# Optimization experiments

Hardware: AMD Instinct MI355X
Metric: run time of the kernel (lower is better)

Reference implementation:

```python
import jax, jax.numpy as jnp
import numpy as np

N = 8192   # nodes in each graph (N1 must equal N2: V is built from x1)
D = 512    # output_dim


def setup_inputs() -> dict:
    key = jax.random.key(0)
    k1, k2, kq, kk, kv = jax.random.split(key, 5)
    std = 1.0 / np.sqrt(D)
    return {
        "x1": jax.random.normal(k1, (N, D), dtype=jnp.float32),
        "x2": jax.random.normal(k2, (N, D), dtype=jnp.float32),
        "q": jax.random.uniform(kq, (D, D), dtype=jnp.float32, minval=-std, maxval=std),
        "k": jax.random.uniform(kk, (D, D), dtype=jnp.float32, minval=-std, maxval=std),
        "v": jax.random.uniform(kv, (D, D), dtype=jnp.float32, minval=-std, maxval=std),
    }


def reference(x1, x2, q, k, v):
    Q = x1 @ q                       # [N, D]
    V = x1 @ v                       # [N, D]  (note: V from x1, as in the original)
    K = x2 @ k                       # [N, D]
    e = jax.nn.leaky_relu(Q @ K.T, negative_slope=0.01)  # [N, N]
    attention = jax.nn.softmax(e, axis=-1)
    return attention @ V             # [N, D]
```

## Files before the change

kernel.cpp:

```cpp
#include <hip/hip_runtime.h>
#include <hip/hip_bf16.h>

typedef unsigned short u16;
typedef unsigned int u32;
typedef float floatx4 __attribute__((ext_vector_type(4)));
typedef _Float16 f16x8 __attribute__((ext_vector_type(8)));

#define NN 8192
#define DD 512
#define NPARTS 4
#define JCHUNK 2048
#define RB_PER_PART 64

__device__ __forceinline__ u16 f2h(float f) {
    _Float16 h = (_Float16)f;
    return __builtin_bit_cast(u16, h);
}
__device__ __forceinline__ float h2f(u16 u) {
    _Float16 h = __builtin_bit_cast(_Float16, u);
    return (float)h;
}

__device__ __forceinline__ void async16(const u16* g, u16* l) {
    __builtin_amdgcn_global_load_lds(
        (const __attribute__((address_space(1))) u32*)g,
        (__attribute__((address_space(3))) u32*)l, 16, 0, 0);
}

__global__ __launch_bounds__(256)
void prep_kernel(const float* __restrict__ x1, const float* __restrict__ x2,
                 const float* __restrict__ qw, const float* __restrict__ kw,
                 const float* __restrict__ vw,
                 u16* __restrict__ x1h, u16* __restrict__ x2h,
                 u16* __restrict__ qT, u16* __restrict__ kT,
                 u16* __restrict__ vT, int* __restrict__ cnt)
{
    const int t = blockIdx.x * 256 + threadIdx.x;
    const int stride = gridDim.x * 256;
    if (t < NPARTS) cnt[t] = 0;

    const int NQ = NN * DD / 4;
    for (int i = t; i < NQ; i += stride) {
        float4 f = ((const float4*)x1)[i];
        ushort4 h;
        h.x = f2h(f.x); h.y = f2h(f.y); h.z = f2h(f.z); h.w = f2h(f.w);
        ((ushort4*)x1h)[i] = h;
        f = ((const float4*)x2)[i];
        h.x = f2h(f.x); h.y = f2h(f.y); h.z = f2h(f.z); h.w = f2h(f.w);
        ((ushort4*)x2h)[i] = h;
    }
    const int NW = DD * DD;
    for (int i = t; i < NW; i += stride) {
        const int k = i >> 9, n = i & 511;
        qT[n * DD + k] = f2h(qw[i]);
        kT[n * DD + k] = f2h(kw[i]);
        vT[n * DD + k] = f2h(vw[i]);
    }
}

__global__ __launch_bounds__(256, 2)
void proj_kernel(const u16* __restrict__ x1h, const u16* __restrict__ x2h,
                 const u16* __restrict__ qT, const u16* __restrict__ kT,
                 const u16* __restrict__ vT,
                 u16* __restrict__ Qf, u16* __restrict__ Kf, u16* __restrict__ VT)
{
    const int which = blockIdx.z;
    const u16* A = (which == 1) ? x2h : x1h;
    const u16* W = (which == 0) ? qT : (which == 1 ? kT : vT);

    __shared__ u16 Ab[2][128 * 64];
    __shared__ u16 Wb[2][128 * 64];

    const int tid  = threadIdx.x;
    const int lane = tid & 63;
    const int wave = tid >> 6;
    const int l15  = lane & 15;
    const int quad = lane >> 4;
    const int wm   = (wave & 1) * 64;
    const int wn   = (wave >> 1) * 64;
    const int m0   = blockIdx.x * 128;
    const int n0   = blockIdx.y * 128;

    const int vrs = lane >> 3;
    const int vch = (lane & 7) ^ vrs;
    int sOff[4];
    for (int i = 0; i < 4; i++) {
        const int c = wave * 4 + i;
        sOff[i] = (c * 8 + vrs) * DD + vch * 8;
    }

    auto stage = [&](int buf, int k0) {
        const u16* a = A + (size_t)m0 * DD + k0;
        const u16* w = W + (size_t)n0 * DD + k0;
        u16* da = &Ab[buf][wave * 2048];
        u16* dw = &Wb[buf][wave * 2048];
        async16(a + sOff[0], da);
        async16(a + sOff[1], da + 512);
        async16(a + sOff[2], da + 1024);
        async16(a + sOff[3], da + 1536);
        async16(w + sOff[0], dw);
        async16(w + sOff[1], dw + 512);
        async16(w + sOff[2], dw + 1024);
        async16(w + sOff[3], dw + 1536);
        __builtin_amdgcn_sched_barrier(0);
    };

    floatx4 acc[4][4] = {};

    stage(0, 0);
    asm volatile("s_waitcnt vmcnt(0)" ::: "memory");
    __syncthreads();

    for (int t = 0; t < 8; t++) {
        if (t < 7) stage((t & 1) ^ 1, (t + 1) * 64);
        const int buf = t & 1;
        __builtin_amdgcn_s_setprio(1);
        for (int ks = 0; ks < 2; ks++) {
            f16x8 af[4], bf[4];
            for (int mi = 0; mi < 4; mi++) {
                const int row = wm + mi * 16 + l15;
                const int ch  = (ks * 4 + quad) ^ (l15 & 7);
                af[mi] = *(const f16x8*)&Ab[buf][row * 64 + ch * 8];
            }
            for (int ni = 0; ni < 4; ni++) {
                const int row = wn + ni * 16 + l15;
                const int ch  = (ks * 4 + quad) ^ (l15 & 7);
                bf[ni] = *(const f16x8*)&Wb[buf][row * 64 + ch * 8];
            }
            for (int mi = 0; mi < 4; mi++)
                for (int ni = 0; ni < 4; ni++)
                    acc[mi][ni] = __builtin_amdgcn_mfma_f32_16x16x32_f16(
                        af[mi], bf[ni], acc[mi][ni], 0, 0, 0);
        }
        __builtin_amdgcn_s_setprio(0);
        asm volatile("s_waitcnt vmcnt(0)" ::: "memory");
        __syncthreads();
    }

    for (int mi = 0; mi < 4; mi++)
        for (int ni = 0; ni < 4; ni++) {
            if (which == 2) {
                const int row0 = m0 + wm + mi * 16 + quad * 4;
                const int col  = n0 + wn + ni * 16 + l15;
                uint2 p;
                p.x = ((u32)f2h(acc[mi][ni][1]) << 16) | f2h(acc[mi][ni][0]);
                p.y = ((u32)f2h(acc[mi][ni][3]) << 16) | f2h(acc[mi][ni][2]);
                *(uint2*)&VT[(size_t)col * NN + row0] = p;
            } else {
                for (int r = 0; r < 4; r++) {
                    const int row = m0 + wm + mi * 16 + quad * 4 + r;
                    const int col = n0 + wn + ni * 16 + l15;
                    const u16 hv = f2h(acc[mi][ni][r]);
                    if (which == 0) Qf[(size_t)row * DD + col] = hv;
                    else            Kf[(size_t)row * DD + col] = hv;
                }
            }
        }
}

__global__ __launch_bounds__(512, 2)
void attn_kernel(const u16* __restrict__ Qf, const u16* __restrict__ Kf,
                 const u16* __restrict__ VT,
                 u16* __restrict__ Opart, float* __restrict__ Mp,
                 float* __restrict__ Lp, int* __restrict__ cnt)
{
    const int tid  = threadIdx.x;
    const int lane = tid & 63;
    const int wave = tid >> 6;
    const int w3   = wave & 3;
    const int wsel = wave >> 2;
    const int l15  = lane & 15;
    const int quad = lane >> 4;

    __shared__ u16 KV[6][8192];
    __shared__ u16 Ps[8][16 * 68];
    __shared__ int sPart, sRb;

    if (tid == 0) {
        u32 xcd;
        asm volatile("s_getreg_b32 %0, hwreg(HW_REG_XCC_ID)" : "=s"(xcd));
        xcd &= 3;
        int part = -1, rb = 0;
        for (int t = 0; t < 4; t++) {
            const int p = (xcd + t) & 3;
            const int idx = atomicAdd(&cnt[p], 1);
            if (idx < RB_PER_PART) { part = p; rb = idx; break; }
        }
        sPart = part; sRb = rb;
    }
    __syncthreads();
    const int part = sPart;
    const int rb   = sRb;
    if (part < 0) return;

    const int q0 = rb * 128 + wave * 16;

    f16x8 qf[16];
    for (int kk = 0; kk < 16; kk++)
        qf[kk] = *(const f16x8*)&Qf[(size_t)(q0 + l15) * DD + kk * 32 + quad * 8];

    floatx4 o[32] = {};
    float m_run[4], l_run[4];
    for (int r = 0; r < 4; r++) { m_run[r] = -1e30f; l_run[r] = 0.f; }

    const int j_begin = part * JCHUNK;
    const int j_end   = j_begin + JCHUNK;

    const int krow4  = lane >> 4;
    const int kpos16 = lane & 15;
    const int vrs    = lane >> 3;
    const int vch    = (lane & 7) ^ vrs;

    int kOff[4], vOff[4];
    for (int i = 0; i < 4; i++) {
        const int c    = w3 * 4 + i;
        const int krow = c * 4 + krow4;
        kOff[i] = krow * DD + (kpos16 ^ (krow & 7)) * 8;
        vOff[i] = (c * 8 + vrs) * NN + vch * 8;
    }

    auto stageK = [&](int dq, int j0, int slot) {
        const u16* b = Kf + (size_t)j0 * DD + dq * 128;
        u16* d = &KV[slot][w3 * 2048];
        async16(b + kOff[0], d);
        async16(b + kOff[1], d + 512);
        async16(b + kOff[2], d + 1024);
        async16(b + kOff[3], d + 1536);
        __builtin_amdgcn_sched_barrier(0);
    };
    auto stageV = [&](int dq, int j0, int slot) {
        const u16* b = VT + (size_t)dq * 128 * NN + j0;
        u16* d = &KV[slot][w3 * 2048];
        async16(b + vOff[0], d);
        async16(b + vOff[1], d + 512);
        async16(b + vOff[2], d + 1024);
        async16(b + vOff[3], d + 1536);
        __builtin_amdgcn_sched_barrier(0);
    };

    auto qkQ = [&](int rg, int dq, floatx4* s) {
        __builtin_amdgcn_s_setprio(1);
        for (int k8 = 0; k8 < 4; k8++)
            for (int nt = 0; nt < 4; nt++) {
                const int row = nt * 16 + l15;
                const int ch  = (k8 * 4 + quad) ^ (l15 & 7);
                f16x8 b = *(const f16x8*)&KV[rg][row * 128 + ch * 8];
                s[nt] = __builtin_amdgcn_mfma_f32_16x16x32_f16(qf[dq * 4 + k8], b, s[nt], 0, 0, 0);
            }
        __builtin_amdgcn_s_setprio(0);
    };
    auto pvQ = [&](int rg, int dq) {
        f16x8 pf0 = *(const f16x8*)&Ps[wave][l15 * 68 + quad * 8];
        f16x8 pf1 = *(const f16x8*)&Ps[wave][l15 * 68 + 32 + quad * 8];
        __builtin_amdgcn_s_setprio(1);
        for (int t = 0; t < 8; t++) {
            const int row = t * 16 + l15;
            const int c0  = quad ^ (l15 & 7);
            const int c1  = (4 + quad) ^ (l15 & 7);
            f16x8 b0 = *(const f16x8*)&KV[rg][row * 64 + c0 * 8];
            f16x8 b1 = *(const f16x8*)&KV[rg][row * 64 + c1 * 8];
            o[dq * 8 + t] = __builtin_amdgcn_mfma_f32_16x16x32_f16(pf0, b0, o[dq * 8 + t], 0, 0, 0);
            o[dq * 8 + t] = __builtin_amdgcn_mfma_f32_16x16x32_f16(pf1, b1, o[dq * 8 + t], 0, 0, 0);
        }
        __builtin_amdgcn_s_setprio(0);
    };

    auto pbar = [&]() {
        asm volatile("s_waitcnt vmcnt(4)" ::: "memory");
        asm volatile("s_barrier" ::: "memory");
    };
    auto wrap6 = [](int x) { return x >= 6 ? x - 6 : x; };

    if (wsel == 0) { stageK(0, j_begin, 0); stageK(2, j_begin, 2); }
    else           { stageK(1, j_begin, 1); stageK(3, j_begin, 3); }
    asm volatile("s_waitcnt vmcnt(0)" ::: "memory");
    asm volatile("s_barrier" ::: "memory");

    int sc = 4;

    for (int j0 = j_begin; j0 < j_end; j0 += 64) {
        const int jn = (j0 + 64 < j_end) ? j0 + 64 : j_begin;
        floatx4 s[4] = {};
        int sA, sB, cA, cB;

        sA = sc; sB = sc + 1; cA = wrap6(sc + 2); cB = cA + 1; sc = cA;
        if (wsel == 0) stageV(0, j0, sA); else stageV(1, j0, sB);
        qkQ(cA, 0, s);
        qkQ(cB, 1, s);
        pbar();

        sA = sc; sB = sc + 1; cA = wrap6(sc + 2); cB = cA + 1; sc = cA;
        if (wsel == 0) stageV(2, j0, sA); else stageV(3, j0, sB);
        qkQ(cA, 2, s);
        qkQ(cB, 3, s);

        for (int nt = 0; nt < 4; nt++)
            for (int r = 0; r < 4; r++) {
                float x = s[nt][r];
                s[nt][r] = x >= 0.f ? x : 0.01f * x;
            }
        float mt4[4];
        for (int r = 0; r < 4; r++)
            mt4[r] = fmaxf(fmaxf(s[0][r], s[1][r]), fmaxf(s[2][r], s[3][r]));
        for (int off = 1; off < 16; off <<= 1)
            for (int r = 0; r < 4; r++)
                mt4[r] = fmaxf(mt4[r], __shfl_xor(mt4[r], off));

        float alpha[4];
        for (int r = 0; r < 4; r++) {
            const float mnew = fmaxf(m_run[r], mt4[r]);
            alpha[r] = __expf(m_run[r] - mnew);
            m_run[r] = mnew;
        }
        float ls[4] = {0.f, 0.f, 0.f, 0.f};
        u16 pv[4][4];
        for (int nt = 0; nt < 4; nt++)
            for (int r = 0; r < 4; r++) {
                const float p = __expf(s[nt][r] - m_run[r]);
                ls[r] += p;
                pv[nt][r] = f2h(p);
            }
        for (int off = 1; off < 16; off <<= 1)
            for (int r = 0; r < 4; r++)
                ls[r] += __shfl_xor(ls[r], off);
        for (int r = 0; r < 4; r++)
            l_run[r] = l_run[r] * alpha[r] + ls[r];
        const bool need = (alpha[0] != 1.f) | (alpha[1] != 1.f) |
                          (alpha[2] != 1.f) | (alpha[3] != 1.f);
        if (__any(need))
            for (int i = 0; i < 32; i++)
                for (int r = 0; r < 4; r++)
                    o[i][r] *= alpha[r];

        for (int nt = 0; nt < 4; nt++)
            for (int r = 0; r < 4; r++)
                Ps[wave][(quad * 4 + r) * 68 + nt * 16 + l15] = pv[nt][r];
        asm volatile("s_waitcnt lgkmcnt(0)" ::: "memory");

        pbar();

        sA = sc; sB = sc + 1; cA = wrap6(sc + 2); cB = cA + 1; sc = cA;
        if (wsel == 0) stageK(0, jn, sA); else stageK(1, jn, sB);
        pvQ(cA, 0);
        pvQ(cB, 1);
        pbar();

        sA = sc; sB = sc + 1; cA = wrap6(sc + 2); cB = cA + 1; sc = cA;
        if (wsel == 0) stageK(2, jn, sA); else stageK(3, jn, sB);
        pvQ(cA, 2);
        pvQ(cB, 3);
        pbar();
    }

    asm volatile("s_waitcnt vmcnt(0)" ::: "memory");

    for (int i = 0; i < 32; i++)
        for (int r = 0; r < 4; r++) {
            const int row = q0 + quad * 4 + r;
            const int col = i * 16 + l15;
            Opart[((size_t)part * NN + row) * DD + col] = f2h(o[i][r]);
        }
    if (l15 == 0)
        for (int r = 0; r < 4; r++) {
            const int row = q0 + quad * 4 + r;
            Mp[part * NN + row] = m_run[r];
            Lp[part * NN + row] = l_run[r];
        }
}

__global__ __launch_bounds__(256)
void combine_kernel(const u16* __restrict__ Opart, const float* __restrict__ Mp,
                    const float* __restrict__ Lp, float* __restrict__ out)
{
    const int t   = blockIdx.x * 256 + threadIdx.x;
    const int row = t >> 6;
    const int c0  = (t & 63) * 8;

    float m[NPARTS], l[NPARTS];
    float M = -1e30f;
    for (int p = 0; p < NPARTS; p++) {
        m[p] = Mp[p * NN + row];
        l[p] = Lp[p * NN + row];
        M = fmaxf(M, m[p]);
    }
    float w[NPARTS], L = 0.f;
    for (int p = 0; p < NPARTS; p++) { w[p] = __expf(m[p] - M); L += w[p] * l[p]; }
    const float inv = 1.f / L;

    float acc[8] = {};
    for (int p = 0; p < NPARTS; p++) {
        f16x8 v = *(const f16x8*)&Opart[((size_t)p * NN + row) * DD + c0];
        for (int j = 0; j < 8; j++)
            acc[j] += w[p] * (float)v[j];
    }
    float4 o0, o1;
    o0.x = acc[0] * inv; o0.y = acc[1] * inv; o0.z = acc[2] * inv; o0.w = acc[3] * inv;
    o1.x = acc[4] * inv; o1.y = acc[5] * inv; o1.z = acc[6] * inv; o1.w = acc[7] * inv;
    *(float4*)&out[(size_t)row * DD + c0]     = o0;
    *(float4*)&out[(size_t)row * DD + c0 + 4] = o1;
}

extern "C" void kernel_launch(void* const* d_in, const int* in_sizes, int n_in,
                              void* d_out, int out_size, void* d_ws, size_t ws_size,
                              hipStream_t stream)
{
    const float* x1 = (const float*)d_in[0];
    const float* x2 = (const float*)d_in[1];
    const float* qw = (const float*)d_in[2];
    const float* kw = (const float*)d_in[3];
    const float* vw = (const float*)d_in[4];
    float* out = (float*)d_out;

    u16* Qf = (u16*)d_ws;
    u16* Kf = Qf + (size_t)NN * DD;
    u16* VT = Kf + (size_t)NN * DD;
    u16* Opart = VT + (size_t)NN * DD;
    float* Mp = (float*)(Opart + (size_t)NPARTS * NN * DD);
    float* Lp = Mp + NPARTS * NN;
    int* cnt = (int*)(Lp + NPARTS * NN);
    u16* x1h = (u16*)(cnt + 8);
    u16* x2h = x1h + (size_t)NN * DD;
    u16* qT  = x2h + (size_t)NN * DD;
    u16* kT  = qT + DD * DD;
    u16* vT  = kT + DD * DD;

    prep_kernel<<<1024, 256, 0, stream>>>(x1, x2, qw, kw, vw,
                                          x1h, x2h, qT, kT, vT, cnt);
    proj_kernel<<<dim3(64, 4, 3), 256, 0, stream>>>(x1h, x2h, qT, kT, vT,
                                                    Qf, Kf, VT);
    attn_kernel<<<dim3(RB_PER_PART * NPARTS), 512, 0, stream>>>(Qf, Kf, VT, Opart, Mp, Lp, cnt);
    combine_kernel<<<(NN * 64) / 256, 256, 0, stream>>>(Opart, Mp, Lp, out);
}
```

Measured before the change: 353.2 us.

## Give each attention wave two 16-row query tiles with 4 waves per block

Shrinks the attention block from 8 waves to 4, each wave now processing 32 query rows (two MFMA M-tiles). Each K/V fragment read from LDS is reused by both tiles, halving LDS read traffic per MFMA. Every wave now stages both halves of each K/V chunk, so the wait count is raised to match. The cost is much higher register pressure (64 output accumulators, 32 Q fragments), fewer waves to hide latency, and a risk of spilling under launch_bounds(256,1).

```diff
diff --git a/kernel.cpp b/kernel.cpp
--- a/kernel.cpp
+++ b/kernel.cpp
@@ -158,7 +158,7 @@
         }
 }
 
-__global__ __launch_bounds__(512, 2)
+__global__ __launch_bounds__(256, 1)
 void attn_kernel(const u16* __restrict__ Qf, const u16* __restrict__ Kf,
                  const u16* __restrict__ VT,
                  u16* __restrict__ Opart, float* __restrict__ Mp,
@@ -167,13 +167,11 @@
     const int tid  = threadIdx.x;
     const int lane = tid & 63;
     const int wave = tid >> 6;
-    const int w3   = wave & 3;
-    const int wsel = wave >> 2;
     const int l15  = lane & 15;
     const int quad = lane >> 4;
 
     __shared__ u16 KV[6][8192];
-    __shared__ u16 Ps[8][16 * 68];
+    __shared__ u16 Ps[4][32 * 68];
     __shared__ int sPart, sRb;
 
     if (tid == 0) {
@@ -193,15 +191,17 @@
     const int rb   = sRb;
     if (part < 0) return;
 
-    const int q0 = rb * 128 + wave * 16;
-
-    f16x8 qf[16];
-    for (int kk = 0; kk < 16; kk++)
-        qf[kk] = *(const f16x8*)&Qf[(size_t)(q0 + l15) * DD + kk * 32 + quad * 8];
-
-    floatx4 o[32] = {};
-    float m_run[4], l_run[4];
-    for (int r = 0; r < 4; r++) { m_run[r] = -1e30f; l_run[r] = 0.f; }
+    const int q0 = rb * 128 + wave * 32;
+
+    f16x8 qf[32];
+    for (int m = 0; m < 2; m++)
+        for (int kk = 0; kk < 16; kk++)
+            qf[m * 16 + kk] = *(const f16x8*)&Qf[(size_t)(q0 + m * 16 + l15) * DD
+                                                 + kk * 32 + quad * 8];
+
+    floatx4 o[64] = {};
+    float m_run[8], l_run[8];
+    for (int i = 0; i < 8; i++) { m_run[i] = -1e30f; l_run[i] = 0.f; }
 
     const int j_begin = part * JCHUNK;
     const int j_end   = j_begin + JCHUNK;
@@ -213,7 +213,7 @@
 
     int kOff[4], vOff[4];
     for (int i = 0; i < 4; i++) {
-        const int c    = w3 * 4 + i;
+        const int c    = wave * 4 + i;
         const int krow = c * 4 + krow4;
         kOff[i] = krow * DD + (kpos16 ^ (krow & 7)) * 8;
         vOff[i] = (c * 8 + vrs) * NN + vch * 8;
@@ -221,7 +221,7 @@
 
     auto stageK = [&](int dq, int j0, int slot) {
         const u16* b = Kf + (size_t)j0 * DD + dq * 128;
-        u16* d = &KV[slot][w3 * 2048];
+        u16* d = &KV[slot][wave * 2048];
         async16(b + kOff[0], d);
         async16(b + kOff[1], d + 512);
         async16(b + kOff[2], d + 1024);
@@ -230,7 +230,7 @@
     };
     auto stageV = [&](int dq, int j0, int slot) {
         const u16* b = VT + (size_t)dq * 128 * NN + j0;
-        u16* d = &KV[slot][w3 * 2048];
+        u16* d = &KV[slot][wave * 2048];
         async16(b + vOff[0], d);
         async16(b + vOff[1], d + 512);
         async16(b + vOff[2], d + 1024);
@@ -245,13 +245,18 @@
                 const int row = nt * 16 + l15;
                 const int ch  = (k8 * 4 + quad) ^ (l15 & 7);
                 f16x8 b = *(const f16x8*)&KV[rg][row * 128 + ch * 8];
-                s[nt] = __builtin_amdgcn_mfma_f32_16x16x32_f16(qf[dq * 4 + k8], b, s[nt], 0, 0, 0);
+                s[nt]     = __builtin_amdgcn_mfma_f32_16x16x32_f16(
+                                qf[dq * 4 + k8], b, s[nt], 0, 0, 0);
+                s[4 + nt] = __builtin_amdgcn_mfma_f32_16x16x32_f16(
+                                qf[16 + dq * 4 + k8], b, s[4 + nt], 0, 0, 0);
             }
         __builtin_amdgcn_s_setprio(0);
     };
     auto pvQ = [&](int rg, int dq) {
-        f16x8 pf0 = *(const f16x8*)&Ps[wave][l15 * 68 + quad * 8];
-        f16x8 pf1 = *(const f16x8*)&Ps[wave][l15 * 68 + 32 + quad * 8];
+        f16x8 pA0 = *(const f16x8*)&Ps[wave][l15 * 68 + quad * 8];
+        f16x8 pA1 = *(const f16x8*)&Ps[wave][l15 * 68 + 32 + quad * 8];
+        f16x8 pB0 = *(const f16x8*)&Ps[wave][(16 + l15) * 68 + quad * 8];
+        f16x8 pB1 = *(const f16x8*)&Ps[wave][(16 + l15) * 68 + 32 + quad * 8];
         __builtin_amdgcn_s_setprio(1);
         for (int t = 0; t < 8; t++) {
             const int row = t * 16 + l15;
@@ -259,20 +264,26 @@
             const int c1  = (4 + quad) ^ (l15 & 7);
             f16x8 b0 = *(const f16x8*)&KV[rg][row * 64 + c0 * 8];
             f16x8 b1 = *(const f16x8*)&KV[rg][row * 64 + c1 * 8];
-            o[dq * 8 + t] = __builtin_amdgcn_mfma_f32_16x16x32_f16(pf0, b0, o[dq * 8 + t], 0, 0, 0);
-            o[dq * 8 + t] = __builtin_amdgcn_mfma_f32_16x16x32_f16(pf1, b1, o[dq * 8 + t], 0, 0, 0);
+            o[dq * 8 + t]      = __builtin_amdgcn_mfma_f32_16x16x32_f16(
+                                     pA0, b0, o[dq * 8 + t], 0, 0, 0);
+            o[dq * 8 + t]      = __builtin_amdgcn_mfma_f32_16x16x32_f16(
+                                     pA1, b1, o[dq * 8 + t], 0, 0, 0);
+            o[32 + dq * 8 + t] = __builtin_amdgcn_mfma_f32_16x16x32_f16(
+                                     pB0, b0, o[32 + dq * 8 + t], 0, 0, 0);
+            o[32 + dq * 8 + t] = __builtin_amdgcn_mfma_f32_16x16x32_f16(
+                                     pB1, b1, o[32 + dq * 8 + t], 0, 0, 0);
         }
         __builtin_amdgcn_s_setprio(0);
     };
 
     auto pbar = [&]() {
-        asm volatile("s_waitcnt vmcnt(4)" ::: "memory");
+        asm volatile("s_waitcnt vmcnt(8)" ::: "memory");
         asm volatile("s_barrier" ::: "memory");
     };
     auto wrap6 = [](int x) { return x >= 6 ? x - 6 : x; };
 
-    if (wsel == 0) { stageK(0, j_begin, 0); stageK(2, j_begin, 2); }
-    else           { stageK(1, j_begin, 1); stageK(3, j_begin, 3); }
+    stageK(0, j_begin, 0); stageK(1, j_begin, 1);
+    stageK(2, j_begin, 2); stageK(3, j_begin, 3);
     asm volatile("s_waitcnt vmcnt(0)" ::: "memory");
     asm volatile("s_barrier" ::: "memory");
 
@@ -280,73 +291,73 @@
 
     for (int j0 = j_begin; j0 < j_end; j0 += 64) {
         const int jn = (j0 + 64 < j_end) ? j0 + 64 : j_begin;
-        floatx4 s[4] = {};
+        floatx4 s[8] = {};
         int sA, sB, cA, cB;
 
         sA = sc; sB = sc + 1; cA = wrap6(sc + 2); cB = cA + 1; sc = cA;
-        if (wsel == 0) stageV(0, j0, sA); else stageV(1, j0, sB);
+        stageV(0, j0, sA); stageV(1, j0, sB);
         qkQ(cA, 0, s);
         qkQ(cB, 1, s);
         pbar();
 
         sA = sc; sB = sc + 1; cA = wrap6(sc + 2); cB = cA + 1; sc = cA;
-        if (wsel == 0) stageV(2, j0, sA); else stageV(3, j0, sB);
+        stageV(2, j0, sA); stageV(3, j0, sB);
         qkQ(cA, 2, s);
         qkQ(cB, 3, s);
 
-        for (int nt = 0; nt < 4; nt++)
+        for (int i = 0; i < 8; i++)
             for (int r = 0; r < 4; r++) {
-                float x = s[nt][r];
-                s[nt][r] = x >= 0.f ? x : 0.01f * x;
-            }
-        float mt4[4];
-        for (int r = 0; r < 4; r++)
-            mt4[r] = fmaxf(fmaxf(s[0][r], s[1][r]), fmaxf(s[2][r], s[3][r]));
+                float x = s[i][r];
+                s[i][r] = x >= 0.f ? x : 0.01f * x;
+            }
+        float mt8[8];
+        for (int m = 0; m < 2; m++)
+            for (int r = 0; r < 4; r++)
+                mt8[m * 4 + r] = fmaxf(fmaxf(s[m * 4 + 0][r], s[m * 4 + 1][r]),
+                                       fmaxf(s[m * 4 + 2][r], s[m * 4 + 3][r]));
         for (int off = 1; off < 16; off <<= 1)
-            for (int r = 0; r < 4; r++)
-                mt4[r] = fmaxf(mt4[r], __shfl_xor(mt4[r], off));
-
-        float alpha[4];
-        for (int r = 0; r < 4; r++) {
-            const float mnew = fmaxf(m_run[r], mt4[r]);
-            alpha[r] = __expf(m_run[r] - mnew);
-            m_run[r] = mnew;
-        }
-        float ls[4] = {0.f, 0.f, 0.f, 0.f};
-        u16 pv[4][4];
-        for (int nt = 0; nt < 4; nt++)
-            for (int r = 0; r < 4; r++) {
-                const float p = __expf(s[nt][r] - m_run[r]);
-                ls[r] += p;
-                pv[nt][r] = f2h(p);
-            }
+            for (int i = 0; i < 8; i++)
+                mt8[i] = fmaxf(mt8[i], __shfl_xor(mt8[i], off));
+
+        float alpha[8];
+        for (int i = 0; i < 8; i++) {
+            const float mnew = fmaxf(m_run[i], mt8[i]);
+            alpha[i] = __expf(m_run[i] - mnew);
+            m_run[i] = mnew;
+        }
+        float ls[8] = {0.f, 0.f, 0.f, 0.f, 0.f, 0.f, 0.f, 0.f};
+        for (int m = 0; m < 2; m++)
+            for (int nt = 0; nt < 4; nt++)
+                for (int r = 0; r < 4; r++) {
+                    const float p = __expf(s[m * 4 + nt][r] - m_run[m * 4 + r]);
+                    ls[m * 4 + r] += p;
+                    Ps[wave][(m * 16 + quad * 4 + r) * 68 + nt * 16 + l15] = f2h(p);
+                }
         for (int off = 1; off < 16; off <<= 1)
-            for (int r = 0; r < 4; r++)
-                ls[r] += __shfl_xor(ls[r], off);
-        for (int r = 0; r < 4; r++)
-            l_run[r] = l_run[r] * alpha[r] + ls[r];
-        const bool need = (alpha[0] != 1.f) | (alpha[1] != 1.f) |
-                          (alpha[2] != 1.f) | (alpha[3] != 1.f);
-        if (__any(need))
-            for (int i = 0; i < 32; i++)
+            for (int i = 0; i < 8; i++)
+                ls[i] += __shfl_xor(ls[i], off);
+        for (int i = 0; i < 8; i++)
+            l_run[i] = l_run[i] * alpha[i] + ls[i];
+        bool need = false;
+        for (int i = 0; i < 8; i++) need |= (alpha[i] != 1.f);
+        if (__any(need)) {
+            #pragma unroll
+            for (int i = 0; i < 64; i++)
                 for (int r = 0; r < 4; r++)
-                    o[i][r] *= alpha[r];
-
-        for (int nt = 0; nt < 4; nt++)
-            for (int r = 0; r < 4; r++)
-                Ps[wave][(quad * 4 + r) * 68 + nt * 16 + l15] = pv[nt][r];
+                    o[i][r] *= alpha[(i >> 5) * 4 + r];
+        }
         asm volatile("s_waitcnt lgkmcnt(0)" ::: "memory");
 
         pbar();
 
         sA = sc; sB = sc + 1; cA = wrap6(sc + 2); cB = cA + 1; sc = cA;
-        if (wsel == 0) stageK(0, jn, sA); else stageK(1, jn, sB);
+        stageK(0, jn, sA); stageK(1, jn, sB);
         pvQ(cA, 0);
         pvQ(cB, 1);
         pbar();
 
         sA = sc; sB = sc + 1; cA = wrap6(sc + 2); cB = cA + 1; sc = cA;
-        if (wsel == 0) stageK(2, jn, sA); else stageK(3, jn, sB);
+        stageK(2, jn, sA); stageK(3, jn, sB);
         pvQ(cA, 2);
         pvQ(cB, 3);
         pbar();
@@ -354,18 +365,21 @@
 
     asm volatile("s_waitcnt vmcnt(0)" ::: "memory");
 
-    for (int i = 0; i < 32; i++)
-        for (int r = 0; r < 4; r++) {
-            const int row = q0 + quad * 4 + r;
-            const int col = i * 16 + l15;
-            Opart[((size_t)part * NN + row) * DD + col] = f2h(o[i][r]);
-        }
+    #pragma unroll
+    for (int m = 0; m < 2; m++)
+        for (int i = 0; i < 32; i++)
+            for (int r = 0; r < 4; r++) {
+                const int row = q0 + m * 16 + quad * 4 + r;
+                const int col = i * 16 + l15;
+                Opart[((size_t)part * NN + row) * DD + col] = f2h(o[m * 32 + i][r]);
+            }
     if (l15 == 0)
-        for (int r = 0; r < 4; r++) {
-            const int row = q0 + quad * 4 + r;
-            Mp[part * NN + row] = m_run[r];
-            Lp[part * NN + row] = l_run[r];
-        }
+        for (int m = 0; m < 2; m++)
+            for (int r = 0; r < 4; r++) {
+                const int row = q0 + m * 16 + quad * 4 + r;
+                Mp[part * NN + row] = m_run[m * 4 + r];
+                Lp[part * NN + row] = l_run[m * 4 + r];
+            }
 }
 
 __global__ __launch_bounds__(256)
@@ -428,6 +442,6 @@
                                           x1h, x2h, qT, kT, vT, cnt);
     proj_kernel<<<dim3(64, 4, 3), 256, 0, stream>>>(x1h, x2h, qT, kT, vT,
                                                     Qf, Kf, VT);
-    attn_kernel<<<dim3(RB_PER_PART * NPARTS), 512, 0, stream>>>(Qf, Kf, VT, Opart, Mp, Lp, cnt);
+    attn_kernel<<<dim3(RB_PER_PART * NPARTS), 256, 0, stream>>>(Qf, Kf, VT, Opart, Mp, Lp, cnt);
     combine_kernel<<<(NN * 64) / 256, 256, 0, stream>>>(Opart, Mp, Lp, out);
 }
```

New measurement: 820.4 us. +132.3%, slower.
